# Kernel tuning notes

Hardware: AMD Instinct MI355X
Metric: run time of the kernel (lower is better)

The kernel has to match this reference:

```python
import jax, jax.numpy as jnp
import numpy as np

D = 768        # embed_dim
H = 12         # num_heads
DEPTH = 12
P = 16         # patch size
IMG = 224
G = IMG // P   # 14 patches per side
NPATCH = G * G # 196
N = NPATCH + 1 # seq len with cls token
MLP = 4 * D    # 3072
NC = 1000      # num_classes
EPS = 1e-6


def _ln(x, w, b):
    m = jnp.mean(x, axis=-1, keepdims=True)
    v = jnp.mean((x - m) ** 2, axis=-1, keepdims=True)
    return (x - m) / jnp.sqrt(v + EPS) * w + b


def setup_inputs() -> dict:
    key = jax.random.key(0)
    ks = jax.random.split(key, 12)
    f = lambda k, s: jax.random.normal(k, s, jnp.float32) * 0.02
    return {
        "x": jax.random.normal(ks[0], (32, 3, IMG, IMG), jnp.float32),
        "patch_w": f(ks[1], (3 * P * P, D)),  # Conv2d(3,768,16,16) as matmul
        "patch_b": jnp.zeros((D,), jnp.float32),
        "cls_token": f(ks[2], (1, 1, D)),
        "pos_embed": f(ks[3], (1, N, D)),
        "ln1_w": jnp.ones((DEPTH, D), jnp.float32),
        "ln1_b": jnp.zeros((DEPTH, D), jnp.float32),
        "qkv_w": f(ks[4], (DEPTH, D, 3 * D)),
        "qkv_b": jnp.zeros((DEPTH, 3 * D), jnp.float32),
        "proj_w": f(ks[5], (DEPTH, D, D)),
        "proj_b": jnp.zeros((DEPTH, D), jnp.float32),
        "ln2_w": jnp.ones((DEPTH, D), jnp.float32),
        "ln2_b": jnp.zeros((DEPTH, D), jnp.float32),
        "fc1_w": f(ks[6], (DEPTH, D, MLP)),
        "fc1_b": jnp.zeros((DEPTH, MLP), jnp.float32),
        "fc2_w": f(ks[7], (DEPTH, MLP, D)),
        "fc2_b": jnp.zeros((DEPTH, D), jnp.float32),
        "normf_w": jnp.ones((D,), jnp.float32),
        "normf_b": jnp.zeros((D,), jnp.float32),
        "head_w": f(ks[8], (D, NC)),
        "head_b": jnp.zeros((NC,), jnp.float32),
    }


def _fwd(x, patch_w, patch_b, cls_token, pos_embed, ln1_w, ln1_b, qkv_w, qkv_b,
         proj_w, proj_b, ln2_w, ln2_b, fc1_w, fc1_b, fc2_w, fc2_b,
         normf_w, normf_b, head_w, head_b):
    B = x.shape[0]
    # Patch embed: equivalent to Conv2d(3, D, kernel=16, stride=16)
    patches = x.reshape(B, 3, G, P, G, P).transpose(0, 2, 4, 1, 3, 5)
    patches = patches.reshape(B, NPATCH, 3 * P * P)
    h = patches @ patch_w + patch_b                       # [B, 196, D]
    cls = jnp.broadcast_to(cls_token, (B, 1, D))
    h = jnp.concatenate([cls, h], axis=1) + pos_embed     # [B, N, D]
    scale = (D // H) ** -0.5

    def block(h, p):
        l1w, l1b, qw, qb, pw, pb, l2w, l2b, f1w, f1b, f2w, f2b = p
        y = _ln(h, l1w, l1b)
        qkv = (y @ qw + qb).reshape(B, N, 3, H, D // H).transpose(2, 0, 3, 1, 4)
        q, k, v = qkv[0], qkv[1], qkv[2]                  # [B, H, N, dh]
        attn = jax.nn.softmax(jnp.einsum('bhnd,bhmd->bhnm', q, k) * scale, axis=-1)
        o = jnp.einsum('bhnm,bhmd->bhnd', attn, v).transpose(0, 2, 1, 3).reshape(B, N, D)
        h = h + (o @ pw + pb)
        y = _ln(h, l2w, l2b)
        h = h + (jax.nn.gelu(y @ f1w + f1b, approximate=False) @ f2w + f2b)
        return h, None

    params = (ln1_w, ln1_b, qkv_w, qkv_b, proj_w, proj_b,
              ln2_w, ln2_b, fc1_w, fc1_b, fc2_w, fc2_b)
    h, _ = jax.lax.scan(block, h, params)
    h = _ln(h, normf_w, normf_b)
    return h[:, 0] @ head_w + head_b                      # [B, 1000]


def reference(x, patch_w, patch_b, cls_token, pos_embed, ln1_w, ln1_b, qkv_w, qkv_b,
              proj_w, proj_b, ln2_w, ln2_b, fc1_w, fc1_b, fc2_w, fc2_b,
              normf_w, normf_b, head_w, head_b):
    return _fwd(x, patch_w, patch_b, cls_token, pos_embed, ln1_w, ln1_b, qkv_w, qkv_b,
                proj_w, proj_b, ln2_w, ln2_b, fc1_w, fc1_b, fc2_w, fc2_b,
                normf_w, normf_b, head_w, head_b)
```

## Files before the change

kernel.cpp:

```cpp
#include <hip/hip_runtime.h>
#include <hip/hip_bf16.h>
#include <type_traits>


#define BV   32
#define DIM  768
#define NHD  12
#define DH   64
#define NSEQ 197
#define NPAT 196
#define MLPD 3072
#define NCLS 1000
#define NLAYER 12

typedef __hip_bfloat16 bf16;
typedef __attribute__((ext_vector_type(8))) short s8v;
typedef __attribute__((ext_vector_type(4))) float f32x4;

#define GLDS16(gp, lp) __builtin_amdgcn_global_load_lds( \
    (const __attribute__((address_space(1))) void*)(gp), \
    (__attribute__((address_space(3))) void*)(lp), 16, 0, 0)

__device__ __forceinline__ short f2bf(float v) {
    return (short)__bfloat16_as_ushort(__float2bfloat16(v));
}

template<int ACT, bool RESID, typename TO>
__global__ __launch_bounds__(256)
void bgemm(const bf16* __restrict__ A, const bf16* __restrict__ B,
           const float* __restrict__ bias, TO* __restrict__ C,
           int M, int N, int K, int lda, int ldb, int ldc)
{
    __shared__ short As[8192];

    int nbx = gridDim.x;
    int nb  = nbx * gridDim.y;
    int bid = blockIdx.y * nbx + blockIdx.x;
    {
        int per = nb >> 3, rem = nb & 7;
        int x = bid & 7, loc = bid >> 3;
        bid = x * per + (x < rem ? x : rem) + loc;
    }
    const int m0 = (bid / nbx) * 128;
    const int n0 = (bid % nbx) * 128;

    const int tid  = threadIdx.x;
    const int wave = tid >> 6;
    const int lane = tid & 63;

    const int c0 = wave * 2, c1 = c0 + 1;
    const int rsub = lane >> 2;
    const int kp8  = (lane & 3) * 8;

    int ra0 = m0 + c0 * 16 + rsub; if (ra0 > M - 1) ra0 = M - 1;
    int ra1 = m0 + c1 * 16 + rsub; if (ra1 > M - 1) ra1 = M - 1;
    int rb0 = n0 + c0 * 16 + rsub; if (rb0 > N - 1) rb0 = N - 1;
    int rb1 = n0 + c1 * 16 + rsub; if (rb1 > N - 1) rb1 = N - 1;

    const bf16* pa0 = A + (long)ra0 * lda + kp8;
    const bf16* pa1 = A + (long)ra1 * lda + kp8;
    const bf16* pb0 = B + (long)rb0 * ldb + kp8;
    const bf16* pb1 = B + (long)rb1 * ldb + kp8;

    const int wm = wave >> 1, wn = wave & 1;
    const int colr = lane & 15;
    const int quad = lane >> 4;

    f32x4 acc[4][4];
    #pragma unroll
    for (int i = 0; i < 4; ++i)
        #pragma unroll
        for (int j = 0; j < 4; ++j)
            acc[i][j] = (f32x4){0.f, 0.f, 0.f, 0.f};

    const short* AsP = &As[(wm * 64 + colr) * 32 + quad * 8];
    const short* BsP = &As[4096 + (wn * 64 + colr) * 32 + quad * 8];

    for (int k0 = 0; k0 < K; k0 += 32) {
        GLDS16(pa0, &As[c0 * 512]);
        GLDS16(pa1, &As[c1 * 512]);
        GLDS16(pb0, &As[4096 + c0 * 512]);
        GLDS16(pb1, &As[4096 + c1 * 512]);
        pa0 += 32; pa1 += 32; pb0 += 32; pb1 += 32;
        __syncthreads();

        s8v a[4], b[4];
        #pragma unroll
        for (int i = 0; i < 4; ++i) a[i] = *(const s8v*)(AsP + i * 512);
        #pragma unroll
        for (int j = 0; j < 4; ++j) b[j] = *(const s8v*)(BsP + j * 512);
        #pragma unroll
        for (int i = 0; i < 4; ++i)
            #pragma unroll
            for (int j = 0; j < 4; ++j)
                acc[i][j] = __builtin_amdgcn_mfma_f32_16x16x32_bf16(
                    a[i], b[j], acc[i][j], 0, 0, 0);
        __syncthreads();
    }

    float* ep = ((float*)As) + wave * 1024;
    const int lrow = lane >> 2;
    const int lc4  = (lane & 3) * 16;

    #pragma unroll
    for (int i = 0; i < 4; ++i) {
        #pragma unroll
        for (int j = 0; j < 4; ++j)
            #pragma unroll
            for (int r = 0; r < 4; ++r)
                ep[(quad * 4 + r) * 64 + j * 16 + colr] = acc[i][j][r];
        __syncthreads();

        int gm = m0 + wm * 64 + i * 16 + lrow;
        int gn = n0 + wn * 64 + lc4;
        if (gm < M) {
            float vals[16];
            #pragma unroll
            for (int c = 0; c < 16; ++c) vals[c] = ep[lrow * 64 + lc4 + c];

            if (gn + 16 <= N) {
                if (bias) {
                    #pragma unroll
                    for (int c = 0; c < 16; ++c) vals[c] += bias[gn + c];
                }
                if (ACT == 1) {
                    #pragma unroll
                    for (int c = 0; c < 16; ++c)
                        vals[c] = 0.5f * vals[c] *
                                  (1.0f + erff(vals[c] * 0.70710678118654752f));
                }
                if constexpr (std::is_same<TO, float>::value) {
                    float* Cp = (float*)C + (long)gm * ldc + gn;
                    if constexpr (RESID) {
                        #pragma unroll
                        for (int c4 = 0; c4 < 4; ++c4) {
                            f32x4 old = *(const f32x4*)&Cp[c4 * 4];
                            #pragma unroll
                            for (int e = 0; e < 4; ++e) vals[c4 * 4 + e] += old[e];
                        }
                    }
                    #pragma unroll
                    for (int c4 = 0; c4 < 4; ++c4) {
                        f32x4 v; 
                        #pragma unroll
                        for (int e = 0; e < 4; ++e) v[e] = vals[c4 * 4 + e];
                        *(f32x4*)&Cp[c4 * 4] = v;
                    }
                } else {
                    short* Cp = (short*)C + (long)gm * ldc + gn;
                    s8v v0, v1;
                    #pragma unroll
                    for (int e = 0; e < 8; ++e) { v0[e] = f2bf(vals[e]); v1[e] = f2bf(vals[8 + e]); }
                    *(s8v*)&Cp[0] = v0;
                    *(s8v*)&Cp[8] = v1;
                }
            } else {
                #pragma unroll
                for (int c = 0; c < 16; ++c) {
                    int g = gn + c;
                    if (g >= N) continue;
                    float v = vals[c];
                    if (bias) v += bias[g];
                    if (ACT == 1) v = 0.5f * v * (1.0f + erff(v * 0.70710678118654752f));
                    long idx = (long)gm * ldc + g;
                    if constexpr (RESID) v += ((const float*)C)[idx];
                    if constexpr (std::is_same<TO, float>::value) C[idx] = v;
                    else C[idx] = __float2bfloat16(v);
                }
            }
        }
        __syncthreads();
    }
}

__global__ __launch_bounds__(256)
void attn_kernel(const bf16* __restrict__ qkv, bf16* __restrict__ O)
{
    __shared__ short Qs[64 * 72];
    __shared__ short Ks[224 * 72];
    __shared__ short Vt[64 * 224];

    const int tid  = threadIdx.x;
    const int wave = tid >> 6;
    const int lane = tid & 63;
    const int q0 = blockIdx.x * 64;
    const int b  = blockIdx.y / NHD;
    const int h  = blockIdx.y % NHD;
    const bf16* base = qkv + (long)b * NSEQ * (3 * DIM);

    #pragma unroll
    for (int p = 0; p < 2; ++p) {
        int idx = p * 2048 + tid * 8;
        int row = idx >> 6, col = idx & 63;
        int gr = q0 + row; if (gr > NSEQ - 1) gr = NSEQ - 1;
        *(s8v*)&Qs[row * 72 + col] =
            *(const s8v*)&base[(long)gr * (3 * DIM) + h * DH + col];
    }
    #pragma unroll
    for (int p = 0; p < 7; ++p) {
        int idx = p * 2048 + tid * 8;
        int row = idx >> 6, col = idx & 63;
        int gr = row; if (gr > NSEQ - 1) gr = NSEQ - 1;
        *(s8v*)&Ks[row * 72 + col] =
            *(const s8v*)&base[(long)gr * (3 * DIM) + DIM + h * DH + col];
    }
    {
        int seqL = tid & 31, dc = tid >> 5;
        #pragma unroll
        for (int st = 0; st < 7; ++st) {
            int seq = st * 32 + seqL;
            int gr = seq; if (gr > NSEQ - 1) gr = NSEQ - 1;
            s8v v = *(const s8v*)&base[(long)gr * (3 * DIM) + 2 * DIM + h * DH + dc * 8];
            #pragma unroll
            for (int i = 0; i < 8; ++i)
                Vt[(dc * 8 + i) * 224 + seq] = v[i];
        }
    }
    __syncthreads();

    const int colr = lane & 15;
    const int quad = lane >> 4;

    f32x4 s[14];
    #pragma unroll
    for (int j = 0; j < 14; ++j) s[j] = (f32x4){0.f, 0.f, 0.f, 0.f};
    #pragma unroll
    for (int kk = 0; kk < 2; ++kk) {
        s8v a = *(const s8v*)&Qs[(wave * 16 + colr) * 72 + quad * 8 + kk * 32];
        #pragma unroll
        for (int j = 0; j < 14; ++j) {
            s8v bf = *(const s8v*)&Ks[(j * 16 + colr) * 72 + quad * 8 + kk * 32];
            s[j] = __builtin_amdgcn_mfma_f32_16x16x32_bf16(a, bf, s[j], 0, 0, 0);
        }
    }

    float mx[4] = {-1e30f, -1e30f, -1e30f, -1e30f};
    #pragma unroll
    for (int j = 0; j < 14; ++j) {
        int c = j * 16 + colr;
        #pragma unroll
        for (int r = 0; r < 4; ++r) {
            s[j][r] *= 0.125f;
            if (c < NSEQ) mx[r] = fmaxf(mx[r], s[j][r]);
        }
    }
    #pragma unroll
    for (int off = 1; off <= 8; off <<= 1)
        #pragma unroll
        for (int r = 0; r < 4; ++r)
            mx[r] = fmaxf(mx[r], __shfl_xor(mx[r], off));

    float sum[4] = {0.f, 0.f, 0.f, 0.f};
    #pragma unroll
    for (int j = 0; j < 14; ++j) {
        int c = j * 16 + colr;
        #pragma unroll
        for (int r = 0; r < 4; ++r) {
            float v = (c < NSEQ) ? expf(s[j][r] - mx[r]) : 0.f;
            s[j][r] = v;
            sum[r] += v;
        }
    }
    #pragma unroll
    for (int off = 1; off <= 8; off <<= 1)
        #pragma unroll
        for (int r = 0; r < 4; ++r)
            sum[r] += __shfl_xor(sum[r], off);
    float inv[4];
    #pragma unroll
    for (int r = 0; r < 4; ++r) inv[r] = 1.0f / sum[r];

    __syncthreads();
    short* P = Ks;
    #pragma unroll
    for (int j = 0; j < 14; ++j)
        #pragma unroll
        for (int r = 0; r < 4; ++r)
            P[(wave * 16 + quad * 4 + r) * 224 + j * 16 + colr] =
                f2bf(s[j][r] * inv[r]);

    f32x4 o[4];
    #pragma unroll
    for (int j2 = 0; j2 < 4; ++j2) o[j2] = (f32x4){0.f, 0.f, 0.f, 0.f};
    #pragma unroll
    for (int ks = 0; ks < 7; ++ks) {
        s8v a = *(const s8v*)&P[(wave * 16 + colr) * 224 + quad * 8 + ks * 32];
        #pragma unroll
        for (int j2 = 0; j2 < 4; ++j2) {
            s8v bf = *(const s8v*)&Vt[(j2 * 16 + colr) * 224 + quad * 8 + ks * 32];
            o[j2] = __builtin_amdgcn_mfma_f32_16x16x32_bf16(a, bf, o[j2], 0, 0, 0);
        }
    }

    #pragma unroll
    for (int j2 = 0; j2 < 4; ++j2)
        #pragma unroll
        for (int r = 0; r < 4; ++r) {
            int qrow = q0 + wave * 16 + quad * 4 + r;
            if (qrow < NSEQ)
                O[((long)b * NSEQ + qrow) * DIM + h * DH + j2 * 16 + colr] =
                    __float2bfloat16(o[j2][r]);
        }
}

__global__ __launch_bounds__(256)
void wconv_kernel(const float* __restrict__ in, bf16* __restrict__ out,
                  int R, int C)
{
    __shared__ float t[32][33];
    int c0 = blockIdx.x * 32, r0 = blockIdx.y * 32;
    int tx = threadIdx.x & 31, ty = threadIdx.x >> 5;
    #pragma unroll
    for (int i = 0; i < 4; ++i) {
        int r = r0 + ty + 8 * i;
        if (r < R && c0 + tx < C) t[ty + 8 * i][tx] = in[(long)r * C + c0 + tx];
    }
    __syncthreads();
    #pragma unroll
    for (int i = 0; i < 4; ++i) {
        int c = c0 + ty + 8 * i;
        int r = r0 + tx;
        if (c < C && r < R) out[(long)c * R + r] = __float2bfloat16(t[tx][ty + 8 * i]);
    }
}

__global__ __launch_bounds__(256)
void ln_kernel(const float* __restrict__ in, long in_stride,
               bf16* __restrict__ out, long out_stride,
               const float* __restrict__ w, const float* __restrict__ b)
{
    long r = blockIdx.x;
    const float* x = in + r * in_stride;
    bf16* y = out + r * out_stride;
    int tid = threadIdx.x;

    float s = 0.f, s2 = 0.f;
    for (int i = tid; i < DIM; i += 256) {
        float v = x[i];
        s += v; s2 += v * v;
    }
    #pragma unroll
    for (int off = 32; off > 0; off >>= 1) {
        s  += __shfl_down(s, off);
        s2 += __shfl_down(s2, off);
    }
    __shared__ float red[2][4];
    int wave = tid >> 6, lane = tid & 63;
    if (lane == 0) { red[0][wave] = s; red[1][wave] = s2; }
    __syncthreads();
    if (tid == 0) {
        float t  = red[0][0] + red[0][1] + red[0][2] + red[0][3];
        float t2 = red[1][0] + red[1][1] + red[1][2] + red[1][3];
        float mean = t / (float)DIM;
        float var  = t2 / (float)DIM - mean * mean;
        red[0][0] = mean;
        red[1][0] = 1.0f / sqrtf(var + 1e-6f);
    }
    __syncthreads();
    float mean = red[0][0], rstd = red[1][0];
    for (int i = tid; i < DIM; i += 256)
        y[i] = __float2bfloat16((x[i] - mean) * rstd * w[i] + b[i]);
}

__global__ __launch_bounds__(256)
void im2col_kernel(const float* __restrict__ x, bf16* __restrict__ out)
{
    long i = (long)blockIdx.x * 256 + threadIdx.x;
    const long total = (long)BV * NPAT * DIM;
    if (i >= total) return;
    int col = (int)(i % DIM);
    long row = i / DIM;
    int c  = col >> 8;
    int py = (col >> 4) & 15;
    int px = col & 15;
    int b  = (int)(row / NPAT);
    int pp = (int)(row % NPAT);
    int gy = pp / 14, gx = pp % 14;
    out[i] = __float2bfloat16(
        x[(((long)(b * 3 + c) * 224 + gy * 16 + py) * 224) + gx * 16 + px]);
}

__global__ __launch_bounds__(256)
void assemble_kernel(const float* __restrict__ tmp, const float* __restrict__ cls,
                     const float* __restrict__ pos, float* __restrict__ h)
{
    long i = (long)blockIdx.x * 256 + threadIdx.x;
    const long total = (long)BV * NSEQ * DIM;
    if (i >= total) return;
    int d = (int)(i % DIM);
    long row = i / DIM;
    int n = (int)(row % NSEQ);
    long b = row / NSEQ;
    float v;
    if (n == 0) v = cls[d];
    else        v = tmp[(b * NPAT + (n - 1)) * DIM + d];
    h[i] = v + pos[(long)n * DIM + d];
}

extern "C" void kernel_launch(void* const* d_in, const int* in_sizes, int n_in,
                              void* d_out, int out_size, void* d_ws, size_t ws_size,
                              hipStream_t stream)
{
    const float* x        = (const float*)d_in[0];
    const float* patch_w  = (const float*)d_in[1];
    const float* patch_b  = (const float*)d_in[2];
    const float* cls_tok  = (const float*)d_in[3];
    const float* pos_emb  = (const float*)d_in[4];
    const float* ln1_w    = (const float*)d_in[5];
    const float* ln1_b    = (const float*)d_in[6];
    const float* qkv_w    = (const float*)d_in[7];
    const float* qkv_b    = (const float*)d_in[8];
    const float* proj_w   = (const float*)d_in[9];
    const float* proj_b   = (const float*)d_in[10];
    const float* ln2_w    = (const float*)d_in[11];
    const float* ln2_b    = (const float*)d_in[12];
    const float* fc1_w    = (const float*)d_in[13];
    const float* fc1_b    = (const float*)d_in[14];
    const float* fc2_w    = (const float*)d_in[15];
    const float* fc2_b    = (const float*)d_in[16];
    const float* normf_w  = (const float*)d_in[17];
    const float* normf_b  = (const float*)d_in[18];
    const float* head_w   = (const float*)d_in[19];
    const float* head_b   = (const float*)d_in[20];
    float* out = (float*)d_out;

    const long M = (long)BV * NSEQ;
    const long MP = (long)BV * NPAT;

    float* h      = (float*)d_ws;
    float* ptmp   = h + 4841472L;
    bf16*  qkv    = (bf16*)(ptmp + 4816896L);
    bf16*  lnout  = qkv + 14524416L;
    bf16*  big    = lnout + 4841472L;
    bf16*  wT     = big + 19365888L;
    bf16*  qkvT = wT;
    bf16*  projT = wT + 1769472L;
    bf16*  fc1T  = wT + 2359296L;
    bf16*  fc2T  = wT + 4718592L;

    dim3 blk(256);

    wconv_kernel<<<dim3(24, 24), blk, 0, stream>>>(patch_w, qkvT, DIM, DIM);
    im2col_kernel<<<dim3((unsigned)((MP * DIM + 255) / 256)), blk, 0, stream>>>(x, big);
    bgemm<0, false, float><<<dim3(6, 49), blk, 0, stream>>>(
        big, qkvT, patch_b, ptmp, (int)MP, DIM, DIM, DIM, DIM, DIM);
    assemble_kernel<<<dim3((unsigned)((M * DIM + 255) / 256)), blk, 0, stream>>>(
        ptmp, cls_tok, pos_emb, h);

    for (int l = 0; l < NLAYER; ++l) {
        wconv_kernel<<<dim3(72, 24), blk, 0, stream>>>(
            qkv_w + (long)l * DIM * 3 * DIM, qkvT, DIM, 3 * DIM);
        wconv_kernel<<<dim3(24, 24), blk, 0, stream>>>(
            proj_w + (long)l * DIM * DIM, projT, DIM, DIM);
        wconv_kernel<<<dim3(96, 24), blk, 0, stream>>>(
            fc1_w + (long)l * DIM * MLPD, fc1T, DIM, MLPD);
        wconv_kernel<<<dim3(24, 96), blk, 0, stream>>>(
            fc2_w + (long)l * MLPD * DIM, fc2T, MLPD, DIM);

        ln_kernel<<<dim3((unsigned)M), blk, 0, stream>>>(
            h, DIM, lnout, DIM, ln1_w + (long)l * DIM, ln1_b + (long)l * DIM);

        bgemm<0, false, bf16><<<dim3(18, 50), blk, 0, stream>>>(
            lnout, qkvT, qkv_b + (long)l * 3 * DIM, qkv,
            (int)M, 3 * DIM, DIM, DIM, DIM, 3 * DIM);

        attn_kernel<<<dim3(4, BV * NHD), blk, 0, stream>>>(qkv, lnout);

        bgemm<0, true, float><<<dim3(6, 50), blk, 0, stream>>>(
            lnout, projT, proj_b + (long)l * DIM, h,
            (int)M, DIM, DIM, DIM, DIM, DIM);

        ln_kernel<<<dim3((unsigned)M), blk, 0, stream>>>(
            h, DIM, lnout, DIM, ln2_w + (long)l * DIM, ln2_b + (long)l * DIM);

        bgemm<1, false, bf16><<<dim3(24, 50), blk, 0, stream>>>(
            lnout, fc1T, fc1_b + (long)l * MLPD, big,
            (int)M, MLPD, DIM, DIM, DIM, MLPD);

        bgemm<0, true, float><<<dim3(6, 50), blk, 0, stream>>>(
            big, fc2T, fc2_b + (long)l * DIM, h,
            (int)M, DIM, MLPD, MLPD, MLPD, DIM);
    }

    ln_kernel<<<dim3(BV), blk, 0, stream>>>(
        h, (long)NSEQ * DIM, lnout, DIM, normf_w, normf_b);

    wconv_kernel<<<dim3(32, 24), blk, 0, stream>>>(head_w, qkvT, DIM, NCLS);
    bgemm<0, false, float><<<dim3(8, 1), blk, 0, stream>>>(
        lnout, qkvT, head_b, out, BV, NCLS, DIM, DIM, DIM, NCLS);
}
```

Measured before the change: 3.876 ms.

## Triple-buffer GEMM LDS tiles with async global-to-LDS prefetch

Changes the bf16 GEMM main loop from a single LDS buffer with load-then-compute to a three-stage ring buffer. Tiles are prefetched two K-steps ahead with global_load_lds, and explicit vmcnt waits replace the full syncthreads. The aim is to hide global memory latency behind MFMA work. LDS use triples to 48KB per block, which may lower occupancy, and correctness depends on the vmcnt counts matching the four loads issued per stage.

```diff
diff --git a/kernel.cpp b/kernel.cpp
--- a/kernel.cpp
+++ b/kernel.cpp
@@ -31,7 +31,7 @@
            const float* __restrict__ bias, TO* __restrict__ C,
            int M, int N, int K, int lda, int ldb, int ldc)
 {
-    __shared__ short As[8192];
+    __shared__ short As[24576];
 
     int nbx = gridDim.x;
     int nb  = nbx * gridDim.y;
@@ -76,27 +76,53 @@
     const short* AsP = &As[(wm * 64 + colr) * 32 + quad * 8];
     const short* BsP = &As[4096 + (wn * 64 + colr) * 32 + quad * 8];
 
-    for (int k0 = 0; k0 < K; k0 += 32) {
-        GLDS16(pa0, &As[c0 * 512]);
-        GLDS16(pa1, &As[c1 * 512]);
-        GLDS16(pb0, &As[4096 + c0 * 512]);
-        GLDS16(pb1, &As[4096 + c1 * 512]);
-        pa0 += 32; pa1 += 32; pb0 += 32; pb1 += 32;
-        __syncthreads();
-
+#define STAGE(bufi) do {                              \
+        int _o = (bufi) * 8192;                       \
+        GLDS16(pa0, &As[_o + c0 * 512]);              \
+        GLDS16(pa1, &As[_o + c1 * 512]);              \
+        GLDS16(pb0, &As[_o + 4096 + c0 * 512]);       \
+        GLDS16(pb1, &As[_o + 4096 + c1 * 512]);       \
+        pa0 += 32; pa1 += 32; pb0 += 32; pb1 += 32;   \
+    } while (0)
+
+    const int nt = K >> 5;
+    STAGE(0);
+    STAGE(1);
+    int cur = 0, nxt = 2;
+
+    for (int t = 0; t < nt; ++t) {
+        if (t + 2 < nt) {
+            STAGE(nxt);
+            nxt = (nxt == 2) ? 0 : nxt + 1;
+            asm volatile("s_waitcnt vmcnt(8)" ::: "memory");
+        } else if (t + 1 < nt) {
+            asm volatile("s_waitcnt vmcnt(4)" ::: "memory");
+        } else {
+            asm volatile("s_waitcnt vmcnt(0)" ::: "memory");
+        }
+        __builtin_amdgcn_s_barrier();
+        asm volatile("" ::: "memory");
+
+        const short* Ab = AsP + cur * 8192;
+        const short* Bb = BsP + cur * 8192;
         s8v a[4], b[4];
         #pragma unroll
-        for (int i = 0; i < 4; ++i) a[i] = *(const s8v*)(AsP + i * 512);
-        #pragma unroll
-        for (int j = 0; j < 4; ++j) b[j] = *(const s8v*)(BsP + j * 512);
+        for (int i = 0; i < 4; ++i) a[i] = *(const s8v*)(Ab + i * 512);
+        #pragma unroll
+        for (int j = 0; j < 4; ++j) b[j] = *(const s8v*)(Bb + j * 512);
         #pragma unroll
         for (int i = 0; i < 4; ++i)
             #pragma unroll
             for (int j = 0; j < 4; ++j)
                 acc[i][j] = __builtin_amdgcn_mfma_f32_16x16x32_bf16(
                     a[i], b[j], acc[i][j], 0, 0, 0);
-        __syncthreads();
-    }
+
+        cur = (cur == 2) ? 0 : cur + 1;
+        asm volatile("" ::: "memory");
+        __builtin_amdgcn_s_barrier();
+        asm volatile("" ::: "memory");
+    }
+#undef STAGE
 
     float* ep = ((float*)As) + wave * 1024;
     const int lrow = lane >> 2;
@@ -141,7 +167,7 @@
                     }
                     #pragma unroll
                     for (int c4 = 0; c4 < 4; ++c4) {
-                        f32x4 v; 
+                        f32x4 v;
                         #pragma unroll
                         for (int e = 0; e < 4; ++e) v[e] = vals[c4 * 4 + e];
                         *(f32x4*)&Cp[c4 * 4] = v;
```

Result: faster. 3.231 ms (-16.6%).
